# Optimization experiments

Measured on AMD Instinct MI355X. Metric: run time of the kernel, lower is better.

The kernel has to match this reference:

```python
import jax, jax.numpy as jnp
import numpy as np

B = 65536   # batch (number of parallel envs)
HID = 64    # GRU hidden / FC width
ACT = 3     # action count


def setup_inputs() -> dict:
    key = jax.random.key(0)
    ks = iter(jax.random.split(key, 64))

    def rn(shape, s=0.1):
        return jax.random.normal(next(ks), shape, dtype=jnp.float32) * s

    inp = {
        "obs": jax.random.uniform(next(ks), (B, 7, 7, 3), dtype=jnp.float32, maxval=10.0),
        "memory": rn((B, 4 * HID), 1.0),
        "conv_w1": rn((16, 3, 2, 2)), "conv_b1": rn((16,)),
        "conv_w2": rn((32, 16, 2, 2)), "conv_b2": rn((32,)),
        "conv_w3": rn((64, 32, 2, 2)), "conv_b3": rn((64,)),
    }
    for g in ("g1", "g2"):
        for l in (0, 1):
            inp[f"{g}_wih{l}"] = rn((3 * HID, HID))
            inp[f"{g}_whh{l}"] = rn((3 * HID, HID))
            inp[f"{g}_bih{l}"] = rn((3 * HID,))
            inp[f"{g}_bhh{l}"] = rn((3 * HID,))
    inp.update({
        "actor_w1": rn((HID, HID)), "actor_b1": rn((HID,)),
        "actor_w2": rn((ACT, HID)), "actor_b2": rn((ACT,)),
        "critic_w1": rn((HID, HID)), "critic_b1": rn((HID,)),
        "critic_w2": rn((1, HID)), "critic_b2": rn((1,)),
    })
    return inp


def _conv(x, w, b):
    # NCHW, OIHW, VALID, stride 1 (matches nn.Conv2d defaults)
    y = jax.lax.conv_general_dilated(x, w, (1, 1), 'VALID',
                                     dimension_numbers=('NCHW', 'OIHW', 'NCHW'))
    return y + b[None, :, None, None]


def _maxpool2(x):
    return jax.lax.reduce_window(x, -jnp.inf, jax.lax.max,
                                 (1, 1, 2, 2), (1, 1, 2, 2), 'VALID')


def _gru_cell(x, h, wih, whh, bih, bhh):
    # PyTorch GRU cell math (gate order: r, z, n)
    gi = x @ wih.T + bih
    gh = h @ whh.T + bhh
    i_r, i_z, i_n = jnp.split(gi, 3, axis=-1)
    h_r, h_z, h_n = jnp.split(gh, 3, axis=-1)
    r = jax.nn.sigmoid(i_r + h_r)
    z = jax.nn.sigmoid(i_z + h_z)
    n = jnp.tanh(i_n + r * h_n)
    return (1.0 - z) * n + z * h


def reference(obs, memory, conv_w1, conv_b1, conv_w2, conv_b2, conv_w3, conv_b3,
              g1_wih0, g1_whh0, g1_bih0, g1_bhh0, g1_wih1, g1_whh1, g1_bih1, g1_bhh1,
              g2_wih0, g2_whh0, g2_bih0, g2_bhh0, g2_wih1, g2_whh1, g2_bih1, g2_bhh1,
              actor_w1, actor_b1, actor_w2, actor_b2,
              critic_w1, critic_b1, critic_w2, critic_b2):
    bsz = memory.shape[0]
    # obs.transpose(1,3).transpose(2,3): NHWC -> NCHW
    x = jnp.transpose(obs, (0, 3, 1, 2))
    x = jax.nn.relu(_conv(x, conv_w1, conv_b1))   # [B,16,6,6]
    x = _maxpool2(x)                              # [B,16,3,3]
    x = jax.nn.relu(_conv(x, conv_w2, conv_b2))   # [B,32,2,2]
    x = jax.nn.relu(_conv(x, conv_w3, conv_b3))   # [B,64,1,1]
    x = x.reshape(bsz, -1)                        # [B,64]

    h1 = memory[:, :2 * HID].reshape(bsz, 2, HID)
    h2 = memory[:, 2 * HID:].reshape(bsz, 2, HID)

    # single-timestep 2-layer GRU #1
    inp = x
    h1_new = []
    for l, (wih, whh, bih, bhh) in enumerate([(g1_wih0, g1_whh0, g1_bih0, g1_bhh0),
                                              (g1_wih1, g1_whh1, g1_bih1, g1_bhh1)]):
        inp = _gru_cell(inp, h1[:, l], wih, whh, bih, bhh)
        h1_new.append(inp)
    mem1 = jnp.stack(h1_new, axis=1).reshape(bsz, 2 * HID)

    # single-timestep 2-layer GRU #2 (input = GRU1 top-layer output)
    h2_new = []
    for l, (wih, whh, bih, bhh) in enumerate([(g2_wih0, g2_whh0, g2_bih0, g2_bhh0),
                                              (g2_wih1, g2_whh1, g2_bih1, g2_bhh1)]):
        inp = _gru_cell(inp, h2[:, l], wih, whh, bih, bhh)
        h2_new.append(inp)
    mem2 = jnp.stack(h2_new, axis=1).reshape(bsz, 2 * HID)

    embedding = inp  # GRU2 top-layer output, [B,64]

    logits = jax.nn.relu(embedding @ actor_w1.T + actor_b1) @ actor_w2.T + actor_b2
    log_probs = jax.nn.log_softmax(logits, axis=1)          # Categorical(logits=log_softmax)
    value = (jax.nn.relu(embedding @ critic_w1.T + critic_b1) @ critic_w2.T + critic_b2)[:, 0]
    memory_out = jnp.concatenate([mem1, mem2], axis=1)      # [B,256]
    return (log_probs, value, memory_out)
```

## Files before the change

kernel.cpp:

```cpp
#include <hip/hip_runtime.h>

#define BATCH 65536
#define NT 256
#define NTG 512
#define MFMA __builtin_amdgcn_mfma_f32_16x16x32_bf16

typedef short bf16x8 __attribute__((ext_vector_type(8)));
typedef float f32x4 __attribute__((ext_vector_type(4)));
typedef unsigned short u16x8 __attribute__((ext_vector_type(8)));

__device__ __forceinline__ float sigmoidf_(float x) { return 1.0f / (1.0f + __expf(-x)); }
__device__ __forceinline__ float tanhf_(float x) { return 2.0f / (1.0f + __expf(-2.0f * x)) - 1.0f; }
__device__ __forceinline__ unsigned short f2b(float f) {
  union { float f; unsigned int u; } v; v.f = f;
  unsigned int r = (v.u + 0x7FFFu + ((v.u >> 16) & 1u)) >> 16;
  return (unsigned short)r;
}
__device__ __forceinline__ float b2f(unsigned short u) {
  return __uint_as_float(((unsigned int)u) << 16);
}
__device__ __forceinline__ bf16x8 cvt8(float4 a, float4 b) {
  union { unsigned short u[8]; bf16x8 v; } t;
  t.u[0] = f2b(a.x); t.u[1] = f2b(a.y); t.u[2] = f2b(a.z); t.u[3] = f2b(a.w);
  t.u[4] = f2b(b.x); t.u[5] = f2b(b.y); t.u[6] = f2b(b.z); t.u[7] = f2b(b.w);
  return t.v;
}

__global__ __launch_bounds__(NT) void k_prep(
    const float* __restrict__ W0, const float* __restrict__ W1,
    const float* __restrict__ W2, const float* __restrict__ W3,
    const float* __restrict__ W4, const float* __restrict__ W5,
    const float* __restrict__ W6, const float* __restrict__ W7,
    const float* __restrict__ bi0, const float* __restrict__ bi1,
    const float* __restrict__ bi2, const float* __restrict__ bi3,
    const float* __restrict__ bh0, const float* __restrict__ bh1,
    const float* __restrict__ bh2, const float* __restrict__ bh3,
    const float* __restrict__ aw1, const float* __restrict__ cw1,
    const float* __restrict__ w3s,
    unsigned short* __restrict__ wsW, unsigned short* __restrict__ wsH,
    unsigned short* __restrict__ wsW3, float* __restrict__ wsB) {
  const int y = blockIdx.y;
  const int i = blockIdx.x * NT + threadIdx.x;
  if (y < 8) {
    if (i >= 12288) return;
    const float* src = (y == 0) ? W0 : (y == 1) ? W1 : (y == 2) ? W2 : (y == 3) ? W3
                     : (y == 4) ? W4 : (y == 5) ? W5 : (y == 6) ? W6 : W7;
    const int c = y >> 1, p = y & 1;
    const int j = i >> 6, k = i & 63;
    const int g = j >> 6, jrow = j & 63;
    const int jt = jrow >> 4, r16i = jrow & 15;
    const int kseg = k >> 5, kgv = (k & 31) >> 3, e = k & 7;
    const int lane = kgv * 16 + r16i;
    const int q = g * 4 + p * 2 + kseg;
    wsW[c * 24576 + ((jt * 12 + q) * 64 + lane) * 8 + e] = f2b(src[i]);
  } else if (y == 8) {
    if (i < 4096) wsH[i] = f2b(aw1[i]);
  } else if (y == 9) {
    if (i < 4096) wsH[4096 + i] = f2b(cw1[i]);
  } else if (y == 10) {
    if (i < 8192) wsW3[i] = f2b(w3s[i]);
  } else {
    const int c = y - 11;
    if (i < 256) {
      const float* bi = (c == 0) ? bi0 : (c == 1) ? bi1 : (c == 2) ? bi2 : bi3;
      const float* bh = (c == 0) ? bh0 : (c == 1) ? bh1 : (c == 2) ? bh2 : bh3;
      const int j = i & 63, g = i >> 6;
      float v = (g == 0) ? bi[j] + bh[j]
              : (g == 1) ? bi[64 + j] + bh[64 + j]
              : (g == 2) ? bi[128 + j] : bh[128 + j];
      wsB[c * 256 + i] = v;
    }
  }
}

__global__ __launch_bounds__(NT) void k_conv1(const float* __restrict__ obs,
                                              const float* __restrict__ w1,
                                              const float* __restrict__ b1,
                                              unsigned short* __restrict__ pooled_t) {
  const int ph = blockIdx.x >> 8;
  const int s = ((blockIdx.x & 255) << 8) + threadIdx.x;
  const float* o = obs + (size_t)s * 147;
  float r[3][21];
#pragma unroll
  for (int rr = 0; rr < 3; ++rr) {
    const float* orow = o + (2 * ph + rr) * 21;
#pragma unroll
    for (int i = 0; i < 21; ++i) r[rr][i] = orow[i];
  }
#pragma unroll 1
  for (int oc = 0; oc < 16; ++oc) {
    float wv[12];
#pragma unroll
    for (int i = 0; i < 12; ++i) wv[i] = w1[oc * 12 + i];
    const float bias = b1[oc];
#pragma unroll
    for (int pw = 0; pw < 3; ++pw) {
      float m = 0.0f;
#pragma unroll
      for (int dh = 0; dh < 2; ++dh)
#pragma unroll
        for (int dw = 0; dw < 2; ++dw) {
          float acc = bias;
#pragma unroll
          for (int kh = 0; kh < 2; ++kh)
#pragma unroll
            for (int kw = 0; kw < 2; ++kw)
#pragma unroll
              for (int c = 0; c < 3; ++c)
                acc += r[dh + kh][(2 * pw + dw + kw) * 3 + c] * wv[c * 4 + kh * 2 + kw];
          m = fmaxf(m, fmaxf(acc, 0.0f));
        }
      pooled_t[(size_t)(oc * 9 + ph * 3 + pw) * BATCH + s] = f2b(m);
    }
  }
}

__global__ __launch_bounds__(NT) void k_conv2(const unsigned short* __restrict__ pooled_t,
                                              const float* __restrict__ w2,
                                              const float* __restrict__ b2,
                                              unsigned short* __restrict__ c2b) {
  const int g = blockIdx.x >> 8;
  const int s = ((blockIdx.x & 255) << 8) + threadIdx.x;
  const int ocb = 16 * g;
  float acc[16][4];
#pragma unroll
  for (int u = 0; u < 16; ++u) {
    const float bb = b2[ocb + u];
    acc[u][0] = bb; acc[u][1] = bb; acc[u][2] = bb; acc[u][3] = bb;
  }
#pragma unroll 1
  for (int ic = 0; ic < 16; ++ic) {
    float p9[9];
#pragma unroll
    for (int p = 0; p < 9; ++p) p9[p] = b2f(pooled_t[(size_t)(ic * 9 + p) * BATCH + s]);
#pragma unroll
    for (int u = 0; u < 16; ++u) {
      float w[4];
#pragma unroll
      for (int i = 0; i < 4; ++i) w[i] = w2[((ocb + u) * 16 + ic) * 4 + i];
#pragma unroll
      for (int oh = 0; oh < 2; ++oh)
#pragma unroll
        for (int ow = 0; ow < 2; ++ow)
          acc[u][oh * 2 + ow] += p9[(oh + 0) * 3 + (ow + 0)] * w[0] +
                                 p9[(oh + 0) * 3 + (ow + 1)] * w[1] +
                                 p9[(oh + 1) * 3 + (ow + 0)] * w[2] +
                                 p9[(oh + 1) * 3 + (ow + 1)] * w[3];
    }
  }
  unsigned short ob[64];
#pragma unroll
  for (int u = 0; u < 16; ++u)
#pragma unroll
    for (int p = 0; p < 4; ++p) ob[u * 4 + p] = f2b(fmaxf(acc[u][p], 0.0f));
#pragma unroll
  for (int i = 0; i < 8; ++i)
    *(u16x8*)(c2b + (size_t)s * 128 + ocb * 4 + 8 * i) = *(const u16x8*)(ob + 8 * i);
}

#define XSTR 88
__global__ __launch_bounds__(NTG, 4) void k_gru(
    const unsigned short* __restrict__ c2b,
    const float* __restrict__ memF,
    const unsigned short* __restrict__ wsW,
    const unsigned short* __restrict__ wsW3,
    const float* __restrict__ wsB,
    const unsigned short* __restrict__ wsH,
    const float* __restrict__ b3,
    const float* __restrict__ ab1, const float* __restrict__ cb1,
    const float* __restrict__ aw2, const float* __restrict__ ab2,
    const float* __restrict__ cw2, const float* __restrict__ cb2,
    float* __restrict__ out) {
  __shared__ unsigned short wlds[24576];
  __shared__ unsigned short xls[128 * XSTR];
  const int tid = threadIdx.x;
  const int lane = tid & 63;
  const int wave = tid >> 6;
  const int r16 = lane & 15;
  const int kg = lane >> 4;
  const int wbase = wave * 16;
  const int m_base = blockIdx.x * 128 + wbase;
  float* outMem = out + (size_t)4 * BATCH;

  float4 wst[6];
  {
    const float4* wsrc = (const float4*)wsW;
#pragma unroll
    for (int r = 0; r < 6; ++r) wst[r] = wsrc[r * NTG + tid];
  }
  bf16x8 a0[4];
  {
    const unsigned short* ap = c2b + (size_t)(m_base + r16) * 128 + kg * 8;
#pragma unroll
    for (int f = 0; f < 4; ++f) a0[f] = *(const bf16x8*)(ap + f * 32);
  }
  float4 hraw[4];
  {
    const float* hp = memF + (size_t)(m_base + r16) * 256 + kg * 8;
    hraw[0] = *(const float4*)(hp);
    hraw[1] = *(const float4*)(hp + 4);
    hraw[2] = *(const float4*)(hp + 32);
    hraw[3] = *(const float4*)(hp + 36);
  }

#pragma unroll
  for (int n = 0; n < 4; ++n) {
    const float bias = b3[n * 16 + r16];
    const unsigned short* bp = wsW3 + (size_t)(n * 16 + r16) * 128 + kg * 8;
    f32x4 q0 = (f32x4)(0.0f);
#pragma unroll
    for (int f = 0; f < 4; ++f) {
      bf16x8 b = *(const bf16x8*)(bp + f * 32);
      q0 = MFMA(a0[f], b, q0, 0, 0, 0);
    }
#pragma unroll
    for (int q = 0; q < 4; ++q)
      xls[(wbase + kg * 4 + q) * XSTR + n * 16 + r16] = f2b(fmaxf(q0[q] + bias, 0.0f));
  }
  {
    float4* wd = (float4*)wlds;
#pragma unroll
    for (int r = 0; r < 6; ++r) wd[r * NTG + tid] = wst[r];
  }
  __syncthreads();

#pragma unroll 1
  for (int c = 0; c < 4; ++c) {
    const int co = c * 64;
    const float* bcp = wsB + c * 256;
    bf16x8 ax0, ax1, ah0, ah1;
    {
      const unsigned short* xp = xls + (wbase + r16) * XSTR + kg * 8;
      ax0 = *(const bf16x8*)(xp);
      ax1 = *(const bf16x8*)(xp + 32);
    }
    ah0 = cvt8(make_float4(hraw[0].x, hraw[0].y, hraw[0].z, hraw[0].w),
               make_float4(hraw[1].x, hraw[1].y, hraw[1].z, hraw[1].w));
    ah1 = cvt8(make_float4(hraw[2].x, hraw[2].y, hraw[2].z, hraw[2].w),
               make_float4(hraw[3].x, hraw[3].y, hraw[3].z, hraw[3].w));
    if (c < 3) {
      const float* hp = memF + (size_t)(m_base + r16) * 256 + (c + 1) * 64 + kg * 8;
      hraw[0] = *(const float4*)(hp);
      hraw[1] = *(const float4*)(hp + 4);
      hraw[2] = *(const float4*)(hp + 32);
      hraw[3] = *(const float4*)(hp + 36);
    }
    const unsigned short* wl = wlds + lane * 8;
#pragma unroll 2
    for (int jt = 0; jt < 4; ++jt) {
      const unsigned short* wjt = wl + jt * 6144;
      bf16x8 xr0 = *(const bf16x8*)(wjt);
      bf16x8 xr1 = *(const bf16x8*)(wjt + 512);
      bf16x8 hr0 = *(const bf16x8*)(wjt + 1024);
      bf16x8 hr1 = *(const bf16x8*)(wjt + 1536);
      bf16x8 xz0 = *(const bf16x8*)(wjt + 2048);
      bf16x8 xz1 = *(const bf16x8*)(wjt + 2560);
      bf16x8 hz0 = *(const bf16x8*)(wjt + 3072);
      bf16x8 hz1 = *(const bf16x8*)(wjt + 3584);
      bf16x8 xn0 = *(const bf16x8*)(wjt + 4096);
      bf16x8 xn1 = *(const bf16x8*)(wjt + 4608);
      bf16x8 hn0 = *(const bf16x8*)(wjt + 5120);
      bf16x8 hn1 = *(const bf16x8*)(wjt + 5632);
      f32x4 sr = (f32x4)(0.0f), sz = (f32x4)(0.0f), sn = (f32x4)(0.0f), tn = (f32x4)(0.0f);
      sr = MFMA(ax0, xr0, sr, 0, 0, 0);
      sr = MFMA(ax1, xr1, sr, 0, 0, 0);
      sr = MFMA(ah0, hr0, sr, 0, 0, 0);
      sr = MFMA(ah1, hr1, sr, 0, 0, 0);
      sz = MFMA(ax0, xz0, sz, 0, 0, 0);
      sz = MFMA(ax1, xz1, sz, 0, 0, 0);
      sz = MFMA(ah0, hz0, sz, 0, 0, 0);
      sz = MFMA(ah1, hz1, sz, 0, 0, 0);
      sn = MFMA(ax0, xn0, sn, 0, 0, 0);
      sn = MFMA(ax1, xn1, sn, 0, 0, 0);
      tn = MFMA(ah0, hn0, tn, 0, 0, 0);
      tn = MFMA(ah1, hn1, tn, 0, 0, 0);
      float ho[4];
      {
        const size_t base = (size_t)(m_base + kg * 4) * 256 + co + jt * 16 + r16;
        ho[0] = memF[base];       ho[1] = memF[base + 256];
        ho[2] = memF[base + 512]; ho[3] = memF[base + 768];
      }
      const float rb = bcp[jt * 16 + r16];
      const float zb = bcp[64 + jt * 16 + r16];
      const float inb = bcp[128 + jt * 16 + r16];
      const float hnb = bcp[192 + jt * 16 + r16];
#pragma unroll
      for (int q = 0; q < 4; ++q) {
        const int sq = m_base + kg * 4 + q;
        const float rg = sigmoidf_(sr[q] + rb);
        const float zg = sigmoidf_(sz[q] + zb);
        const float ng = tanhf_((sn[q] + inb) + rg * (tn[q] + hnb));
        const float nh = (1.0f - zg) * ng + zg * ho[q];
        outMem[(size_t)sq * 256 + co + jt * 16 + r16] = nh;
        xls[(wbase + kg * 4 + q) * XSTR + jt * 16 + r16] = f2b(nh);
      }
    }
    if (c < 3) {
      __syncthreads();
      const float4* wsrc = (const float4*)(wsW + (size_t)(c + 1) * 24576);
      float4* wd = (float4*)wlds;
#pragma unroll
      for (int r = 0; r < 6; ++r) wd[r * NTG + tid] = wsrc[r * NTG + tid];
      __syncthreads();
    }
  }

  bf16x8 ex0, ex1;
  {
    const unsigned short* xp = xls + (wbase + r16) * XSTR + kg * 8;
    ex0 = *(const bf16x8*)(xp);
    ex1 = *(const bf16x8*)(xp + 32);
  }
  f32x4 ha[8];
#pragma unroll
  for (int n = 0; n < 8; ++n) ha[n] = (f32x4)(0.0f);
#pragma unroll
  for (int n = 0; n < 8; ++n) {
    const unsigned short* wp = wsH + (size_t)(n * 16 + r16) * 64 + kg * 8;
    bf16x8 b0 = *(const bf16x8*)(wp);
    bf16x8 b1 = *(const bf16x8*)(wp + 32);
    ha[n] = MFMA(ex0, b0, ha[n], 0, 0, 0);
    ha[n] = MFMA(ex1, b1, ha[n], 0, 0, 0);
  }
  float w2a0[4], w2a1[4], w2a2[4], w2cc[4], bav[4], bcv[4];
#pragma unroll
  for (int t = 0; t < 4; ++t) {
    const int j = 16 * t + r16;
    w2a0[t] = aw2[j]; w2a1[t] = aw2[64 + j]; w2a2[t] = aw2[128 + j];
    w2cc[t] = cw2[j]; bav[t] = ab1[j]; bcv[t] = cb1[j];
  }
  const float b20 = ab2[0], b21 = ab2[1], b22 = ab2[2], b2c = cb2[0];
#pragma unroll
  for (int q = 0; q < 4; ++q) {
    float l0 = 0.0f, l1 = 0.0f, l2 = 0.0f, vv = 0.0f;
#pragma unroll
    for (int t = 0; t < 4; ++t) {
      const float av = fmaxf(ha[t][q] + bav[t], 0.0f);
      const float cv = fmaxf(ha[t + 4][q] + bcv[t], 0.0f);
      l0 += av * w2a0[t]; l1 += av * w2a1[t]; l2 += av * w2a2[t];
      vv += cv * w2cc[t];
    }
#pragma unroll
    for (int m = 1; m < 16; m <<= 1) {
      l0 += __shfl_xor(l0, m); l1 += __shfl_xor(l1, m);
      l2 += __shfl_xor(l2, m); vv += __shfl_xor(vv, m);
    }
    if (r16 == 0) {
      const int sq = m_base + kg * 4 + q;
      const float g0 = l0 + b20, g1 = l1 + b21, g2 = l2 + b22;
      const float mx = fmaxf(g0, fmaxf(g1, g2));
      const float lse = mx + __logf(__expf(g0 - mx) + __expf(g1 - mx) + __expf(g2 - mx));
      out[(size_t)sq * 3 + 0] = g0 - lse;
      out[(size_t)sq * 3 + 1] = g1 - lse;
      out[(size_t)sq * 3 + 2] = g2 - lse;
      out[(size_t)3 * BATCH + sq] = vv + b2c;
    }
  }
}

extern "C" void kernel_launch(void* const* d_in, const int* in_sizes, int n_in,
                              void* d_out, int out_size, void* d_ws, size_t ws_size,
                              hipStream_t stream) {
  (void)in_sizes; (void)n_in; (void)out_size; (void)ws_size;
  const float* obs = (const float*)d_in[0];
  const float* mem = (const float*)d_in[1];
  const float* w1 = (const float*)d_in[2];
  const float* b1 = (const float*)d_in[3];
  const float* w2 = (const float*)d_in[4];
  const float* b2 = (const float*)d_in[5];
  const float* w3 = (const float*)d_in[6];
  const float* b3 = (const float*)d_in[7];
  const float* gw[16];
  for (int i = 0; i < 16; ++i) gw[i] = (const float*)d_in[8 + i];
  const float* aw1 = (const float*)d_in[24];
  const float* ab1 = (const float*)d_in[25];
  const float* aw2 = (const float*)d_in[26];
  const float* ab2 = (const float*)d_in[27];
  const float* cw1 = (const float*)d_in[28];
  const float* cb1 = (const float*)d_in[29];
  const float* cw2 = (const float*)d_in[30];
  const float* cb2 = (const float*)d_in[31];

  float* out = (float*)d_out;

  unsigned short* pooled_t = (unsigned short*)d_ws;
  unsigned short* c2b = pooled_t + (size_t)144 * BATCH;
  unsigned short* wsW = c2b + (size_t)128 * BATCH;
  unsigned short* wsH = wsW + 98304;
  unsigned short* wsW3 = wsH + 8192;
  float* wsB = (float*)(wsW3 + 8192);

  const dim3 blk(NT);
  hipLaunchKernelGGL(k_prep, dim3(48, 15), blk, 0, stream,
                     gw[0], gw[1], gw[4], gw[5], gw[8], gw[9], gw[12], gw[13],
                     gw[2], gw[6], gw[10], gw[14],
                     gw[3], gw[7], gw[11], gw[15],
                     aw1, cw1, w3, wsW, wsH, wsW3, wsB);
  hipLaunchKernelGGL(k_conv1, dim3(768), blk, 0, stream, obs, w1, b1, pooled_t);
  hipLaunchKernelGGL(k_conv2, dim3(512), blk, 0, stream, pooled_t, w2, b2, c2b);
  hipLaunchKernelGGL(k_gru, dim3(BATCH / 128), dim3(NTG), 0, stream,
                     c2b, mem, wsW, wsW3, wsB, wsH, b3,
                     ab1, cb1, aw2, ab2, cw2, cb2, out);
}
```

Measured before the change: 126.1 us.

## Fuse conv1 and conv2 into one kernel staging obs and pooled maps in LDS

Merges the two conv kernels into one. Each block loads 64 samples' observations with coalesced float4 reads into LDS, computes conv1+pool into an LDS buffer using three of its four waves, then all four waves compute conv2 from LDS. This removes the global round trip of the transposed pooled intermediate and one kernel launch, and replaces strided per-thread obs reads with coalesced loads. The cost is one idle wave during conv1, two block barriers, and about 56KB of LDS per block, which may limit how many blocks fit on a CU.

Result: faster. 110.0 us (-12.8%).

```diff
diff --git a/kernel.cpp b/kernel.cpp
--- a/kernel.cpp
+++ b/kernel.cpp
@@ -73,89 +73,111 @@
   }
 }
 
-__global__ __launch_bounds__(NT) void k_conv1(const float* __restrict__ obs,
-                                              const float* __restrict__ w1,
-                                              const float* __restrict__ b1,
-                                              unsigned short* __restrict__ pooled_t) {
-  const int ph = blockIdx.x >> 8;
-  const int s = ((blockIdx.x & 255) << 8) + threadIdx.x;
-  const float* o = obs + (size_t)s * 147;
-  float r[3][21];
-#pragma unroll
-  for (int rr = 0; rr < 3; ++rr) {
-    const float* orow = o + (2 * ph + rr) * 21;
-#pragma unroll
-    for (int i = 0; i < 21; ++i) r[rr][i] = orow[i];
-  }
+#define OSTR 149
+#define PSTR 146
+__global__ __launch_bounds__(NT) void k_conv12(const float* __restrict__ obs,
+                                               const float* __restrict__ w1,
+                                               const float* __restrict__ b1,
+                                               const float* __restrict__ w2,
+                                               const float* __restrict__ b2,
+                                               unsigned short* __restrict__ c2b) {
+  __shared__ float obs_f[64 * OSTR];
+  __shared__ unsigned short pooled[64 * PSTR];
+  const int tid = threadIdx.x;
+  const int lane = tid & 63;
+  const int wave = tid >> 6;
+  const int m_base = blockIdx.x * 64;
+
+  {
+    const float4* src = (const float4*)(obs + (size_t)m_base * 147);
 #pragma unroll 1
-  for (int oc = 0; oc < 16; ++oc) {
-    float wv[12];
-#pragma unroll
-    for (int i = 0; i < 12; ++i) wv[i] = w1[oc * 12 + i];
-    const float bias = b1[oc];
-#pragma unroll
-    for (int pw = 0; pw < 3; ++pw) {
-      float m = 0.0f;
-#pragma unroll
-      for (int dh = 0; dh < 2; ++dh)
-#pragma unroll
-        for (int dw = 0; dw < 2; ++dw) {
-          float acc = bias;
-#pragma unroll
-          for (int kh = 0; kh < 2; ++kh)
-#pragma unroll
-            for (int kw = 0; kw < 2; ++kw)
-#pragma unroll
-              for (int c = 0; c < 3; ++c)
-                acc += r[dh + kh][(2 * pw + dw + kw) * 3 + c] * wv[c * 4 + kh * 2 + kw];
-          m = fmaxf(m, fmaxf(acc, 0.0f));
-        }
-      pooled_t[(size_t)(oc * 9 + ph * 3 + pw) * BATCH + s] = f2b(m);
-    }
-  }
-}
-
-__global__ __launch_bounds__(NT) void k_conv2(const unsigned short* __restrict__ pooled_t,
-                                              const float* __restrict__ w2,
-                                              const float* __restrict__ b2,
-                                              unsigned short* __restrict__ c2b) {
-  const int g = blockIdx.x >> 8;
-  const int s = ((blockIdx.x & 255) << 8) + threadIdx.x;
-  const int ocb = 16 * g;
-  float acc[16][4];
-#pragma unroll
-  for (int u = 0; u < 16; ++u) {
-    const float bb = b2[ocb + u];
-    acc[u][0] = bb; acc[u][1] = bb; acc[u][2] = bb; acc[u][3] = bb;
-  }
+    for (int i = tid; i < 2352; i += NT) {
+      const float4 v = src[i];
+      int idx = i * 4;
+      int s = idx / 147;
+      int c = idx - s * 147;
+      obs_f[s * OSTR + c] = v.x;
+      if (++c == 147) { c = 0; ++s; } obs_f[s * OSTR + c] = v.y;
+      if (++c == 147) { c = 0; ++s; } obs_f[s * OSTR + c] = v.z;
+      if (++c == 147) { c = 0; ++s; } obs_f[s * OSTR + c] = v.w;
+    }
+  }
+  __syncthreads();
+
+  if (wave < 3) {
+    const int ph = wave, s = lane;
+    float r[3][21];
+#pragma unroll
+    for (int rr = 0; rr < 3; ++rr)
+#pragma unroll
+      for (int i = 0; i < 21; ++i) r[rr][i] = obs_f[s * OSTR + (2 * ph + rr) * 21 + i];
 #pragma unroll 1
-  for (int ic = 0; ic < 16; ++ic) {
-    float p9[9];
-#pragma unroll
-    for (int p = 0; p < 9; ++p) p9[p] = b2f(pooled_t[(size_t)(ic * 9 + p) * BATCH + s]);
-#pragma unroll
-    for (int u = 0; u < 16; ++u) {
-      float w[4];
-#pragma unroll
-      for (int i = 0; i < 4; ++i) w[i] = w2[((ocb + u) * 16 + ic) * 4 + i];
-#pragma unroll
-      for (int oh = 0; oh < 2; ++oh)
-#pragma unroll
-        for (int ow = 0; ow < 2; ++ow)
-          acc[u][oh * 2 + ow] += p9[(oh + 0) * 3 + (ow + 0)] * w[0] +
-                                 p9[(oh + 0) * 3 + (ow + 1)] * w[1] +
-                                 p9[(oh + 1) * 3 + (ow + 0)] * w[2] +
-                                 p9[(oh + 1) * 3 + (ow + 1)] * w[3];
-    }
-  }
-  unsigned short ob[64];
-#pragma unroll
-  for (int u = 0; u < 16; ++u)
-#pragma unroll
-    for (int p = 0; p < 4; ++p) ob[u * 4 + p] = f2b(fmaxf(acc[u][p], 0.0f));
-#pragma unroll
-  for (int i = 0; i < 8; ++i)
-    *(u16x8*)(c2b + (size_t)s * 128 + ocb * 4 + 8 * i) = *(const u16x8*)(ob + 8 * i);
+    for (int oc = 0; oc < 16; ++oc) {
+      float wv[12];
+#pragma unroll
+      for (int i = 0; i < 12; ++i) wv[i] = w1[oc * 12 + i];
+      const float bias = b1[oc];
+#pragma unroll
+      for (int pw = 0; pw < 3; ++pw) {
+        float m = 0.0f;
+#pragma unroll
+        for (int dh = 0; dh < 2; ++dh)
+#pragma unroll
+          for (int dw = 0; dw < 2; ++dw) {
+            float acc = bias;
+#pragma unroll
+            for (int kh = 0; kh < 2; ++kh)
+#pragma unroll
+              for (int kw = 0; kw < 2; ++kw)
+#pragma unroll
+                for (int c = 0; c < 3; ++c)
+                  acc += r[dh + kh][(2 * pw + dw + kw) * 3 + c] * wv[c * 4 + kh * 2 + kw];
+            m = fmaxf(m, fmaxf(acc, 0.0f));
+          }
+        pooled[s * PSTR + oc * 9 + ph * 3 + pw] = f2b(m);
+      }
+    }
+  }
+  __syncthreads();
+
+  {
+    const int g = wave, s = lane;
+    const int ocb = g * 8;
+    float acc[8][4];
+#pragma unroll
+    for (int u = 0; u < 8; ++u) {
+      const float bb = b2[ocb + u];
+      acc[u][0] = bb; acc[u][1] = bb; acc[u][2] = bb; acc[u][3] = bb;
+    }
+#pragma unroll 1
+    for (int ic = 0; ic < 16; ++ic) {
+      float p9[9];
+#pragma unroll
+      for (int p = 0; p < 9; ++p) p9[p] = b2f(pooled[s * PSTR + ic * 9 + p]);
+#pragma unroll
+      for (int u = 0; u < 8; ++u) {
+        float w[4];
+#pragma unroll
+        for (int i = 0; i < 4; ++i) w[i] = w2[((ocb + u) * 16 + ic) * 4 + i];
+#pragma unroll
+        for (int oh = 0; oh < 2; ++oh)
+#pragma unroll
+          for (int ow = 0; ow < 2; ++ow)
+            acc[u][oh * 2 + ow] += p9[(oh + 0) * 3 + (ow + 0)] * w[0] +
+                                   p9[(oh + 0) * 3 + (ow + 1)] * w[1] +
+                                   p9[(oh + 1) * 3 + (ow + 0)] * w[2] +
+                                   p9[(oh + 1) * 3 + (ow + 1)] * w[3];
+      }
+    }
+    unsigned short ob[32];
+#pragma unroll
+    for (int u = 0; u < 8; ++u)
+#pragma unroll
+      for (int p = 0; p < 4; ++p) ob[u * 4 + p] = f2b(fmaxf(acc[u][p], 0.0f));
+#pragma unroll
+    for (int i = 0; i < 4; ++i)
+      *(u16x8*)(c2b + (size_t)(m_base + s) * 128 + g * 32 + 8 * i) = *(const u16x8*)(ob + 8 * i);
+  }
 }
 
 #define XSTR 88
@@ -383,8 +405,7 @@
 
   float* out = (float*)d_out;
 
-  unsigned short* pooled_t = (unsigned short*)d_ws;
-  unsigned short* c2b = pooled_t + (size_t)144 * BATCH;
+  unsigned short* c2b = (unsigned short*)d_ws;
   unsigned short* wsW = c2b + (size_t)128 * BATCH;
   unsigned short* wsH = wsW + 98304;
   unsigned short* wsW3 = wsH + 8192;
@@ -396,8 +417,8 @@
                      gw[2], gw[6], gw[10], gw[14],
                      gw[3], gw[7], gw[11], gw[15],
                      aw1, cw1, w3, wsW, wsH, wsW3, wsB);
-  hipLaunchKernelGGL(k_conv1, dim3(768), blk, 0, stream, obs, w1, b1, pooled_t);
-  hipLaunchKernelGGL(k_conv2, dim3(512), blk, 0, stream, pooled_t, w2, b2, c2b);
+  hipLaunchKernelGGL(k_conv12, dim3(BATCH / 64), blk, 0, stream,
+                     obs, w1, b1, w2, b2, c2b);
   hipLaunchKernelGGL(k_gru, dim3(BATCH / 128), dim3(NTG), 0, stream,
                      c2b, mem, wsW, wsW3, wsB, wsH, b3,
                      ab1, cb1, aw2, ab2, cw2, cb2, out);
```
